# Kernel optimization log

Hardware: AMD Instinct MI355X
Metric: run time of the kernel (lower is better)

The kernel has to match this reference:

```python
import jax, jax.numpy as jnp
import numpy as np

B, S, D, H = 2, 2048, 2048, 16
HD = D // H  # head_dim = 128


def setup_inputs() -> dict:
    key = jax.random.key(0)
    ks = jax.random.split(key, 7)
    s = 0.02
    return {
        "q": jax.random.normal(ks[0], (B, S, D), jnp.float32),
        "k": jax.random.normal(ks[1], (B, S, D), jnp.float32),
        "v": jax.random.normal(ks[2], (B, S, D), jnp.float32),
        "wq": jax.random.normal(ks[3], (D, D), jnp.float32) * s,
        "wk": jax.random.normal(ks[4], (D, D), jnp.float32) * s,
        "wv": jax.random.normal(ks[5], (D, D), jnp.float32) * s,
        "wo": jax.random.normal(ks[6], (D, D), jnp.float32) * s,
    }


def reference(q, k, v, wq, wk, wv, wo):
    # Linear(bias=False): y = x @ W.T  (torch weight layout [out, in])
    xq = jnp.einsum("bse,me->bsm", q, wq).reshape(B, S, H, HD).transpose(0, 2, 1, 3)
    xk = jnp.einsum("bse,me->bsm", k, wk).reshape(B, S, H, HD).transpose(0, 2, 1, 3)
    xv = jnp.einsum("bse,me->bsm", v, wv).reshape(B, S, H, HD).transpose(0, 2, 1, 3)
    scores = jnp.einsum("bhqd,bhkd->bhqk", xq, xk) / jnp.sqrt(jnp.float32(HD))
    # causal mask: -inf above diagonal
    causal = jnp.tril(jnp.ones((S, S), dtype=bool))
    scores = jnp.where(causal[None, None], scores, jnp.float32(-jnp.inf))
    probs = jax.nn.softmax(scores.astype(jnp.float32), axis=-1)
    out = jnp.einsum("bhqk,bhkd->bhqd", probs, xv)  # [B,H,S,HD]
    out = out.transpose(0, 2, 1, 3).reshape(B, S, D)
    out = jnp.einsum("bsm,em->bse", out, wo)
    return out
```

## Files before the change

kernel.cpp:

```cpp
#include <hip/hip_runtime.h>

typedef __bf16 bf16x8 __attribute__((ext_vector_type(8)));
typedef float f32x4 __attribute__((ext_vector_type(4)));

__device__ inline unsigned short f2bf(float f) {
  unsigned int u = __float_as_uint(f);
  u = (u + 0x7FFFu + ((u >> 16) & 1u)) >> 16;
  return (unsigned short)u;
}

__device__ inline void gl_lds16(const void* g, void* l) {
  __builtin_amdgcn_global_load_lds(
      (__attribute__((address_space(1))) const void*)g,
      (__attribute__((address_space(3))) void*)l, 16, 0, 0);
}

__global__ __launch_bounds__(256) void cvt_batch(const float* __restrict__ p0,
                                                 const float* __restrict__ p1,
                                                 const float* __restrict__ p2,
                                                 const float* __restrict__ p3,
                                                 unsigned short* __restrict__ out,
                                                 int n4each) {
  const int y = blockIdx.y;
  const float* src = (y == 0) ? p0 : (y == 1) ? p1 : (y == 2) ? p2 : p3;
  unsigned short* dst = out + (size_t)y * n4each * 4;
  int i = blockIdx.x * 256 + threadIdx.x;
  if (i >= n4each) return;
  const float4 v = ((const float4*)src)[i];
  ushort4 o;
  o.x = f2bf(v.x); o.y = f2bf(v.y); o.z = f2bf(v.z); o.w = f2bf(v.w);
  ((ushort4*)dst)[i] = o;
}

template <int MODE>
__global__ __launch_bounds__(512, 2) void gemm8(const unsigned short* __restrict__ A,
                                                const unsigned short* __restrict__ Wb,
                                                void* __restrict__ Cv,
                                                int N, int Kloop, int lda,
                                                float qscale) {
  extern __shared__ char lds[];
  const int tid = threadIdx.x;
  const int w = tid >> 6, l = tid & 63;
  const int wr = w >> 2, wc = w & 3;

  const int nbx = N >> 8;
  const int cpx = gridDim.x >> 3;
  const int bid = blockIdx.x;
  const int swz = (bid & 7) * cpx + (bid >> 3);
  const int by = swz / nbx, bx = swz % nbx;
  const int m0 = by << 7, n0 = bx << 8;

  const unsigned short* W = Wb;
  const unsigned short* Ab = A;
  float scale = 1.0f;
  int seg = 0;
  if (MODE == 0) {
    seg = m0 >> 12;
    W = Wb + (size_t)seg * 2048 * 2048;
    scale = (seg == 0) ? qscale : 1.0f;
  }

  const int col_l = ((l & 3) * 8) ^ ((l >= 32) ? 16 : 0);
  const size_t rowA0 = (size_t)(m0 + w * 16 + (l >> 2)) * lda + col_l;
  const size_t rowB0 = (size_t)(n0 + w * 16 + (l >> 2)) * lda + col_l;
  const size_t rowB1 = rowB0 + (size_t)128 * lda;
  const int stA = w * 2048;

  const int Sread = ((l & 15) * 64 + (l >> 4) * 16) ^ ((l & 8) << 2);
  const int ldsAr = Sread;
  const int ldsBr = 16384 + (wc >> 1) * 16384 + Sread;

  const f32x4 fz = {0.f, 0.f, 0.f, 0.f};
  f32x4 acc[4][4];
#pragma unroll
  for (int i = 0; i < 4; i++)
#pragma unroll
    for (int j = 0; j < 4; j++) acc[i][j] = fz;
  bf16x8 af[2][2], bfr[2][4];

#define STAGE_A(b, kb)                                        \
  gl_lds16(Ab + rowA0 + (kb), lds + (b) * 49152 + stA);       \
  gl_lds16(Ab + rowA0 + (kb) + 32, lds + (b) * 49152 + stA + 1024)

#define STAGE_B(b, h, kb)                                                 \
  gl_lds16(W + ((h) ? rowB1 : rowB0) + (kb),                              \
           lds + (b) * 49152 + 16384 + (h) * 16384 + stA);                \
  gl_lds16(W + ((h) ? rowB1 : rowB0) + (kb) + 32,                         \
           lds + (b) * 49152 + 16384 + (h) * 16384 + stA + 1024)

#define LDA(b, qi)                                                             \
  _Pragma("unroll") for (int i = 0; i < 2; ++i) {                              \
    af[0][i] = *(const bf16x8*)(lds + (b) * 49152 + ldsAr +                    \
                                (wr * 4 + (qi) * 2 + i) * 2048);               \
    af[1][i] = *(const bf16x8*)(lds + (b) * 49152 + ldsAr +                    \
                                (wr * 4 + (qi) * 2 + i) * 2048 + 1024);        \
  }

#define LDB(b, qj)                                                             \
  _Pragma("unroll") for (int j = 0; j < 2; ++j) {                              \
    bfr[0][(qj) * 2 + j] = *(const bf16x8*)(lds + (b) * 49152 + ldsBr +        \
                                            ((wc & 1) * 4 + (qj) * 2 + j) *    \
                                                2048);                         \
    bfr[1][(qj) * 2 + j] = *(const bf16x8*)(lds + (b) * 49152 + ldsBr +        \
                                            ((wc & 1) * 4 + (qj) * 2 + j) *    \
                                                2048 +                         \
                                            1024);                             \
  }

#define MM(qi, qj)                                                             \
  _Pragma("unroll") for (int ks = 0; ks < 2; ++ks)                             \
      _Pragma("unroll") for (int i = 0; i < 2; ++i)                            \
          _Pragma("unroll") for (int j = 0; j < 2; ++j)                        \
              acc[(qi) * 2 + i][(qj) * 2 + j] =                                \
      __builtin_amdgcn_mfma_f32_16x16x32_bf16(af[ks][i], bfr[ks][(qj) * 2 + j],\
                                              acc[(qi) * 2 + i][(qj) * 2 + j], \
                                              0, 0, 0)

#define BAR                      \
  __builtin_amdgcn_s_barrier(); \
  __builtin_amdgcn_sched_barrier(0)
#define WL0                                          \
  asm volatile("s_waitcnt lgkmcnt(0)" ::: "memory"); \
  __builtin_amdgcn_sched_barrier(0)
#define WV4                                         \
  asm volatile("s_waitcnt vmcnt(4)" ::: "memory"); \
  __builtin_amdgcn_sched_barrier(0)
#define PRIO1 __builtin_amdgcn_s_setprio(1)
#define PRIO0 __builtin_amdgcn_s_setprio(0)

  STAGE_A(0, 0);
  STAGE_B(0, 0, 0);
  STAGE_B(0, 1, 0);
  STAGE_B(1, 0, 64);
  STAGE_B(1, 1, 64);
  WV4;
  BAR;

  const int NT = Kloop >> 6;
  const int NI = NT >> 1;
  for (int it = 0; it < NI; ++it) {
    const int t1k = (2 * it + 1) * 64;
    const int t2k = ((2 * it + 2) < NT ? (2 * it + 2) : 0) * 64;
    const int t3k = ((2 * it + 3) < NT ? (2 * it + 3) : 1) * 64;

    LDA(0, 0);
    LDB(0, 0);
    LDB(0, 1);
    STAGE_A(1, t1k);
    BAR; WL0;
    PRIO1; MM(0, 0); MM(0, 1); PRIO0;
    BAR;
    LDA(0, 1);
    STAGE_B(0, 0, t2k);
    STAGE_B(0, 1, t2k);
    BAR; WL0;
    PRIO1; MM(1, 1); MM(1, 0); PRIO0;
    WV4;
    BAR;
    LDA(1, 0);
    LDB(1, 0);
    LDB(1, 1);
    STAGE_A(0, t2k);
    BAR; WL0;
    PRIO1; MM(0, 0); MM(0, 1); PRIO0;
    BAR;
    LDA(1, 1);
    STAGE_B(1, 0, t3k);
    STAGE_B(1, 1, t3k);
    BAR; WL0;
    PRIO1; MM(1, 1); MM(1, 0); PRIO0;
    WV4;
    BAR;
  }
  asm volatile("s_waitcnt vmcnt(0)" ::: "memory");
  __builtin_amdgcn_sched_barrier(0);

  const int erow = m0 + wr * 64 + (l >> 4) * 4;
  const int ecol = n0 + wc * 64 + (l & 15);
  if (MODE == 0) {
    unsigned short* C = (unsigned short*)Cv;
    if (seg == 2) {
      const int b = (m0 - 8192) >> 11;
      const int s0 = ((m0 - 8192) & 2047) + wr * 64 + ((l >> 4) << 2);
      unsigned short* VT = C + (size_t)2 * 4096 * 2048;
#pragma unroll
      for (int i = 0; i < 4; i++)
#pragma unroll
        for (int j = 0; j < 4; j++) {
          const int c = ecol + j * 16;
          ushort4 o;
          o.x = f2bf(acc[i][j][0]); o.y = f2bf(acc[i][j][1]);
          o.z = f2bf(acc[i][j][2]); o.w = f2bf(acc[i][j][3]);
          *(ushort4*)&VT[((size_t)((b << 4) + (c >> 7)) * 128 + (c & 127)) * 2048 +
                         s0 + i * 16] = o;
        }
    } else {
#pragma unroll
      for (int i = 0; i < 4; i++)
#pragma unroll
        for (int j = 0; j < 4; j++)
#pragma unroll
          for (int r = 0; r < 4; r++)
            C[(size_t)(erow + i * 16 + r) * N + ecol + j * 16] =
                f2bf(acc[i][j][r] * scale);
    }
  } else {
    float* C = (float*)Cv;
#pragma unroll
    for (int i = 0; i < 4; i++)
#pragma unroll
      for (int j = 0; j < 4; j++)
#pragma unroll
        for (int r = 0; r < 4; r++)
          C[(size_t)(erow + i * 16 + r) * N + ecol + j * 16] = acc[i][j][r];
  }
#undef STAGE_A
#undef STAGE_B
#undef LDA
#undef LDB
#undef MM
#undef BAR
#undef WL0
#undef WV4
#undef PRIO1
#undef PRIO0
}

__global__ __launch_bounds__(256) void flash_attn(const unsigned short* __restrict__ Qb,
                                                  const unsigned short* __restrict__ Kb,
                                                  const unsigned short* __restrict__ Vt,
                                                  unsigned short* __restrict__ Ob) {
  extern __shared__ char flds[];
  const int h = blockIdx.x, b = blockIdx.y;
  const int tile = 31 - blockIdx.z;
  const int q0 = tile * 64;
  const int tid = threadIdx.x;
  const int w = tid >> 6, l = tid & 63;
  const int lm = l & 15, lk = l >> 4;

  bf16x8 qf[4];
  {
    const unsigned short* qr = Qb + (size_t)(b * 2048 + q0 + w * 16 + lm) * 2048 + h * 128;
    for (int dc = 0; dc < 4; dc++) qf[dc] = *(const bf16x8*)&qr[dc * 32 + lk * 8];
  }

  const f32x4 fz = {0.f, 0.f, 0.f, 0.f};
  float l_r[4] = {0.f, 0.f, 0.f, 0.f};
  f32x4 oacc[8];
  for (int jd = 0; jd < 8; jd++) oacc[jd] = fz;

  const int nkt = tile + 1;
  unsigned short* Pw = (unsigned short*)(flds + 65536) + w * 1024;

#define FSTAGE(kti, bi)                                                              \
  do {                                                                               \
    const int kt_ = (kti)*64;                                                        \
    unsigned short* kls = (unsigned short*)(flds + (bi)*16384);                      \
    unsigned short* vls = (unsigned short*)(flds + 32768 + (bi)*16384);              \
    for (int iss = 0; iss < 4; iss++)                                                \
      gl_lds16(Kb + (size_t)(b * 2048 + kt_ + w * 16 + lm) * 2048 + h * 128 +        \
                   (iss * 4 + lk) * 8,                                               \
               kls + (w * 16 + iss * 4) * 128);                                      \
    for (int t = 0; t < 2; t++) {                                                    \
      int dg = w * 2 + t;                                                            \
      for (int c = 0; c < 2; c++)                                                    \
        gl_lds16(Vt + (size_t)((b * 16 + h) * 128 + dg * 16 + lm) * 2048 + kt_ +     \
                     (c * 4 + lk) * 8,                                               \
                 vls + (dg * 8 + c * 4) * 128);                                      \
    }                                                                                \
  } while (0)

#define FBAR                     \
  __builtin_amdgcn_s_barrier(); \
  __builtin_amdgcn_sched_barrier(0)

  FSTAGE(0, 0);
  if (nkt > 1) FSTAGE(1, 1);
  asm volatile("s_waitcnt vmcnt(0)" ::: "memory");
  __builtin_amdgcn_sched_barrier(0);
  FBAR;

  for (int kti = 0; kti < nkt; kti++) {
    const int cur = kti & 1;
    const int kt = kti * 64;
    const unsigned short* lsKc = (const unsigned short*)(flds + cur * 16384);
    const unsigned short* lsVc = (const unsigned short*)(flds + 32768 + cur * 16384);

    f32x4 s[4];
    for (int jn = 0; jn < 4; jn++) s[jn] = fz;
    __builtin_amdgcn_s_setprio(1);
    for (int jn = 0; jn < 4; jn++)
      for (int dc = 0; dc < 4; dc++) {
        bf16x8 kf = *(const bf16x8*)&lsKc[(jn * 16 + dc * 4) * 128 + l * 8];
        s[jn] = __builtin_amdgcn_mfma_f32_16x16x32_bf16(qf[dc], kf, s[jn], 0, 0, 0);
      }
    __builtin_amdgcn_s_setprio(0);

    const int diag = (kt == q0);
    for (int jn = 0; jn < 4; jn++) {
      int kcol = kt + jn * 16 + lm;
      for (int r = 0; r < 4; r++) {
        int qrow = q0 + w * 16 + lk * 4 + r;
        float p = (diag && kcol > qrow) ? 0.0f : __expf(s[jn][r]);
        s[jn][r] = p;
        l_r[r] += p;
      }
    }

    for (int jn = 0; jn < 4; jn++)
      for (int r = 0; r < 4; r++)
        Pw[(jn * 2 + (lm >> 3)) * 128 + (lk * 4 + r) * 8 + (lm & 7)] = f2bf(s[jn][r]);

    __builtin_amdgcn_s_setprio(1);
    for (int c = 0; c < 2; c++) {
      bf16x8 pf = *(const bf16x8*)&Pw[c * 512 + l * 8];
      for (int jd = 0; jd < 8; jd++) {
        bf16x8 vf = *(const bf16x8*)&lsVc[(jd * 8 + c * 4) * 128 + l * 8];
        oacc[jd] = __builtin_amdgcn_mfma_f32_16x16x32_bf16(pf, vf, oacc[jd], 0, 0, 0);
      }
    }
    __builtin_amdgcn_s_setprio(0);

    FBAR;
    if (kti + 2 < nkt) {
      FSTAGE(kti + 2, cur);
      asm volatile("s_waitcnt vmcnt(8)" ::: "memory");
    } else {
      asm volatile("s_waitcnt vmcnt(0)" ::: "memory");
    }
    __builtin_amdgcn_sched_barrier(0);
    FBAR;
  }

  for (int r = 0; r < 4; r++)
    for (int off = 1; off < 16; off <<= 1) l_r[r] += __shfl_xor(l_r[r], off, 64);

  for (int jd = 0; jd < 8; jd++) {
    int dcol = h * 128 + jd * 16 + lm;
    for (int r = 0; r < 4; r++) {
      size_t idx = (size_t)(b * 2048 + q0 + w * 16 + lk * 4 + r) * 2048 + dcol;
      Ob[idx] = f2bf(oacc[jd][r] / l_r[r]);
    }
  }
#undef FSTAGE
#undef FBAR
}

extern "C" void kernel_launch(void* const* d_in, const int* in_sizes, int n_in,
                              void* d_out, int out_size, void* d_ws, size_t ws_size,
                              hipStream_t stream) {
  const float* q  = (const float*)d_in[0];
  const float* k  = (const float*)d_in[1];
  const float* v  = (const float*)d_in[2];
  const float* wq = (const float*)d_in[3];
  const float* wk = (const float*)d_in[4];
  const float* wv = (const float*)d_in[5];
  const float* wo = (const float*)d_in[6];
  float* out = (float*)d_out;

  static bool attr_done = false;
  if (!attr_done) {
    hipFuncSetAttribute((const void*)gemm8<0>,
                        hipFuncAttributeMaxDynamicSharedMemorySize, 98304);
    hipFuncSetAttribute((const void*)gemm8<1>,
                        hipFuncAttributeMaxDynamicSharedMemorySize, 98304);
    hipFuncSetAttribute((const void*)flash_attn,
                        hipFuncAttributeMaxDynamicSharedMemorySize, 73728);
    attr_done = true;
  }

  const size_t SD = (size_t)4096 * 2048;
  const size_t DD = (size_t)2048 * 2048;
  unsigned short* ws  = (unsigned short*)d_ws;
  unsigned short* qb  = ws;
  unsigned short* wqb = qb + 3 * SD;
  unsigned short* wob = wqb + 3 * DD;
  unsigned short* Qb  = wqb + 4 * DD;
  unsigned short* Kb  = Qb + SD;
  unsigned short* VT  = Kb + SD;
  unsigned short* Ob  = qb + SD;

  cvt_batch<<<dim3(8192, 3), 256, 0, stream>>>(q, k, v, q, qb, (int)(SD / 4));
  cvt_batch<<<dim3(4096, 4), 256, 0, stream>>>(wq, wk, wv, wo, wqb, (int)(DD / 4));

  gemm8<0><<<dim3(768), 512, 98304, stream>>>(qb, wqb, (void*)Qb, 2048, 2048,
                                              2048, 0.08838834764831845f);

  flash_attn<<<dim3(16, 2, 32), 256, 73728, stream>>>(Qb, Kb, VT, Ob);

  gemm8<1><<<dim3(256), 512, 98304, stream>>>(Ob, wob, (void*)out, 2048, 2048,
                                              2048, 1.0f);
}
```

Baseline: 403.1 us.

## Switch GEMM LDS pipeline from double to triple buffering

The GEMM kernel now uses three 48KB LDS stages in rotation instead of two, staging the tile two iterations ahead and waiting on vmcnt(6) instead of vmcnt(4). The aim is to hide more global-to-LDS load latency behind the MFMA work. The price is 144KB of LDS per workgroup, which can reduce how many blocks fit on a CU, and the loop is no longer manually unrolled by two, so pointer rotation adds register and scalar overhead.

```diff
diff --git a/kernel.cpp b/kernel.cpp
--- a/kernel.cpp
+++ b/kernel.cpp
@@ -78,33 +78,29 @@
     for (int j = 0; j < 4; j++) acc[i][j] = fz;
   bf16x8 af[2][2], bfr[2][4];
 
-#define STAGE_A(b, kb)                                        \
-  gl_lds16(Ab + rowA0 + (kb), lds + (b) * 49152 + stA);       \
-  gl_lds16(Ab + rowA0 + (kb) + 32, lds + (b) * 49152 + stA + 1024)
-
-#define STAGE_B(b, h, kb)                                                 \
+#define STAGE_A(pb, kb)                               \
+  gl_lds16(Ab + rowA0 + (kb), (pb) + stA);            \
+  gl_lds16(Ab + rowA0 + (kb) + 32, (pb) + stA + 1024)
+
+#define STAGE_B(pb, h, kb)                                                \
   gl_lds16(W + ((h) ? rowB1 : rowB0) + (kb),                              \
-           lds + (b) * 49152 + 16384 + (h) * 16384 + stA);                \
+           (pb) + 16384 + (h) * 16384 + stA);                             \
   gl_lds16(W + ((h) ? rowB1 : rowB0) + (kb) + 32,                         \
-           lds + (b) * 49152 + 16384 + (h) * 16384 + stA + 1024)
-
-#define LDA(b, qi)                                                             \
+           (pb) + 16384 + (h) * 16384 + stA + 1024)
+
+#define LDA(pb, qi)                                                            \
   _Pragma("unroll") for (int i = 0; i < 2; ++i) {                              \
-    af[0][i] = *(const bf16x8*)(lds + (b) * 49152 + ldsAr +                    \
-                                (wr * 4 + (qi) * 2 + i) * 2048);               \
-    af[1][i] = *(const bf16x8*)(lds + (b) * 49152 + ldsAr +                    \
-                                (wr * 4 + (qi) * 2 + i) * 2048 + 1024);        \
-  }
-
-#define LDB(b, qj)                                                             \
+    af[0][i] = *(const bf16x8*)((pb) + ldsAr + (wr * 4 + (qi) * 2 + i) * 2048);\
+    af[1][i] = *(const bf16x8*)((pb) + ldsAr + (wr * 4 + (qi) * 2 + i) * 2048 +\
+                                1024);                                         \
+  }
+
+#define LDB(pb, qj)                                                            \
   _Pragma("unroll") for (int j = 0; j < 2; ++j) {                              \
-    bfr[0][(qj) * 2 + j] = *(const bf16x8*)(lds + (b) * 49152 + ldsBr +        \
-                                            ((wc & 1) * 4 + (qj) * 2 + j) *    \
-                                                2048);                         \
-    bfr[1][(qj) * 2 + j] = *(const bf16x8*)(lds + (b) * 49152 + ldsBr +        \
-                                            ((wc & 1) * 4 + (qj) * 2 + j) *    \
-                                                2048 +                         \
-                                            1024);                             \
+    bfr[0][(qj) * 2 + j] = *(const bf16x8*)(                                   \
+        (pb) + ldsBr + ((wc & 1) * 4 + (qj) * 2 + j) * 2048);                  \
+    bfr[1][(qj) * 2 + j] = *(const bf16x8*)(                                   \
+        (pb) + ldsBr + ((wc & 1) * 4 + (qj) * 2 + j) * 2048 + 1024);           \
   }
 
 #define MM(qi, qj)                                                             \
@@ -122,55 +118,47 @@
 #define WL0                                          \
   asm volatile("s_waitcnt lgkmcnt(0)" ::: "memory"); \
   __builtin_amdgcn_sched_barrier(0)
-#define WV4                                         \
-  asm volatile("s_waitcnt vmcnt(4)" ::: "memory"); \
+#define WV6                                         \
+  asm volatile("s_waitcnt vmcnt(6)" ::: "memory"); \
   __builtin_amdgcn_sched_barrier(0)
 #define PRIO1 __builtin_amdgcn_s_setprio(1)
 #define PRIO0 __builtin_amdgcn_s_setprio(0)
 
-  STAGE_A(0, 0);
-  STAGE_B(0, 0, 0);
-  STAGE_B(0, 1, 0);
-  STAGE_B(1, 0, 64);
-  STAGE_B(1, 1, 64);
-  WV4;
+  char* p0 = lds;
+  char* p1 = lds + 49152;
+  char* p2 = lds + 98304;
+
+  STAGE_A(p0, 0);
+  STAGE_B(p0, 0, 0);
+  STAGE_B(p0, 1, 0);
+  STAGE_A(p1, 64);
+  STAGE_B(p1, 0, 64);
+  STAGE_B(p1, 1, 64);
+  WV6;
   BAR;
 
   const int NT = Kloop >> 6;
-  const int NI = NT >> 1;
-  for (int it = 0; it < NI; ++it) {
-    const int t1k = (2 * it + 1) * 64;
-    const int t2k = ((2 * it + 2) < NT ? (2 * it + 2) : 0) * 64;
-    const int t3k = ((2 * it + 3) < NT ? (2 * it + 3) : 1) * 64;
-
-    LDA(0, 0);
-    LDB(0, 0);
-    LDB(0, 1);
-    STAGE_A(1, t1k);
+  for (int it = 0; it < NT; ++it) {
+    int t2 = it + 2;
+    if (t2 >= NT) t2 -= NT;
+    const int tk2 = t2 * 64;
+
+    LDA(p0, 0);
+    LDB(p0, 0);
+    LDB(p0, 1);
+    STAGE_A(p2, tk2);
     BAR; WL0;
     PRIO1; MM(0, 0); MM(0, 1); PRIO0;
     BAR;
-    LDA(0, 1);
-    STAGE_B(0, 0, t2k);
-    STAGE_B(0, 1, t2k);
+    LDA(p0, 1);
+    STAGE_B(p2, 0, tk2);
+    STAGE_B(p2, 1, tk2);
     BAR; WL0;
     PRIO1; MM(1, 1); MM(1, 0); PRIO0;
-    WV4;
+    WV6;
     BAR;
-    LDA(1, 0);
-    LDB(1, 0);
-    LDB(1, 1);
-    STAGE_A(0, t2k);
-    BAR; WL0;
-    PRIO1; MM(0, 0); MM(0, 1); PRIO0;
-    BAR;
-    LDA(1, 1);
-    STAGE_B(1, 0, t3k);
-    STAGE_B(1, 1, t3k);
-    BAR; WL0;
-    PRIO1; MM(1, 1); MM(1, 0); PRIO0;
-    WV4;
-    BAR;
+
+    char* tp = p0; p0 = p1; p1 = p2; p2 = tp;
   }
   asm volatile("s_waitcnt vmcnt(0)" ::: "memory");
   __builtin_amdgcn_sched_barrier(0);
@@ -221,7 +209,7 @@
 #undef MM
 #undef BAR
 #undef WL0
-#undef WV4
+#undef WV6
 #undef PRIO1
 #undef PRIO0
 }
@@ -361,9 +349,9 @@
   static bool attr_done = false;
   if (!attr_done) {
     hipFuncSetAttribute((const void*)gemm8<0>,
-                        hipFuncAttributeMaxDynamicSharedMemorySize, 98304);
+                        hipFuncAttributeMaxDynamicSharedMemorySize, 147456);
     hipFuncSetAttribute((const void*)gemm8<1>,
-                        hipFuncAttributeMaxDynamicSharedMemorySize, 98304);
+                        hipFuncAttributeMaxDynamicSharedMemorySize, 147456);
     hipFuncSetAttribute((const void*)flash_attn,
                         hipFuncAttributeMaxDynamicSharedMemorySize, 73728);
     attr_done = true;
@@ -383,11 +371,11 @@
   cvt_batch<<<dim3(8192, 3), 256, 0, stream>>>(q, k, v, q, qb, (int)(SD / 4));
   cvt_batch<<<dim3(4096, 4), 256, 0, stream>>>(wq, wk, wv, wo, wqb, (int)(DD / 4));
 
-  gemm8<0><<<dim3(768), 512, 98304, stream>>>(qb, wqb, (void*)Qb, 2048, 2048,
-                                              2048, 0.08838834764831845f);
+  gemm8<0><<<dim3(768), 512, 147456, stream>>>(qb, wqb, (void*)Qb, 2048, 2048,
+                                               2048, 0.08838834764831845f);
 
   flash_attn<<<dim3(16, 2, 32), 256, 73728, stream>>>(Qb, Kb, VT, Ob);
 
-  gemm8<1><<<dim3(256), 512, 98304, stream>>>(Ob, wob, (void*)out, 2048, 2048,
-                                              2048, 1.0f);
-}
+  gemm8<1><<<dim3(256), 512, 147456, stream>>>(Ob, wob, (void*)out, 2048, 2048,
+                                               2048, 1.0f);
+}
```

Result: slower. 415.5 us (+3.1%).
